# Performance work log

Measured on AMD Instinct MI355X. Metric: run time of the kernel, lower is better.

The kernel has to match this reference:

```python
import jax, jax.numpy as jnp
import numpy as np

N, E, C1, E2, C2, B = 30000, 400000, 15000, 100000, 7500, 16
FV, FE, NC = 6, 3, 10


def _lin(k, i, o):
    kw, kb = jax.random.split(k)
    s = 1.0 / np.sqrt(i)
    w = jax.random.uniform(kw, (i, o), jnp.float32, -s, s)
    b = jax.random.uniform(kb, (o,), jnp.float32, -s, s)
    return w, b


def setup_inputs() -> dict:
    key = jax.random.key(0)
    ks = jax.random.split(key, 20)
    inp = {}
    inp["x"] = jax.random.normal(ks[0], (N, FV), jnp.float32)
    inp["edge_attr"] = jax.random.uniform(ks[1], (E, FE), jnp.float32)
    inp["pos"] = jax.random.uniform(ks[2], (N, 3), jnp.float32)
    inp["edge_index"] = jax.random.randint(ks[3], (2, E), 0, N)
    inp["batch"] = jnp.sort(jax.random.randint(ks[4], (N,), 0, B))
    inp["cluster1"] = jax.random.randint(ks[5], (N,), 0, C1)
    inp["edge_index2"] = jax.random.randint(ks[6], (2, E2), 0, C1)
    inp["cluster2"] = jax.random.randint(ks[7], (C1,), 0, C2)
    inp["w1a"], inp["b1a"] = _lin(ks[8], FE, 25)
    inp["w1b"], inp["b1b"] = _lin(ks[9], 25, 32 * FV)
    inp["root1"] = jax.random.normal(ks[10], (FV, 32), jnp.float32) / np.sqrt(FV)
    inp["bias1"] = jnp.zeros((32,), jnp.float32)
    inp["w2a"], inp["b2a"] = _lin(ks[11], 3, 25)
    inp["w2b"], inp["b2b"] = _lin(ks[12], 25, 32 * 64)
    inp["root2"] = jax.random.normal(ks[13], (32, 64), jnp.float32) / np.sqrt(32)
    inp["bias2"] = jnp.zeros((64,), jnp.float32)
    inp["fc1_w"], inp["fc1_b"] = _lin(ks[14], 64, 128)
    inp["fc2_w"], inp["fc2_b"] = _lin(ks[15], 128, NC)
    return inp


def _seg_mean(v, idx, n):
    s = jax.ops.segment_sum(v, idx, num_segments=n)
    c = jax.ops.segment_sum(jnp.ones(idx.shape, v.dtype), idx, num_segments=n)
    return s / jnp.maximum(c, 1.0)[:, None]


def _seg_max(v, idx, n):
    m = jax.ops.segment_max(v, idx, num_segments=n)
    return jnp.where(jnp.isfinite(m), m, 0.0)  # empty clusters -> 0


def _nnconv(x, src, dst, ea, wa, ba, wb, bb, root, bias, n, ci, co):
    # per-edge weight matrix from edge MLP: [E, ci, co]
    W = (jax.nn.relu(ea @ wa + ba) @ wb + bb).reshape(-1, ci, co)
    msg = jnp.einsum('ei,eio->eo', x[src], W)  # gather + per-edge matmul
    return _seg_mean(msg, dst, n) + x @ root + bias  # scatter-mean + root


def _cartesian(pos, src, dst):
    cart = pos[src] - pos[dst]
    return cart / (2.0 * jnp.max(jnp.abs(cart))) + 0.5  # T.Cartesian(norm=True)


def reference(x, edge_attr, pos, w1a, b1a, w1b, b1b, root1, bias1,
              w2a, b2a, w2b, b2b, root2, bias2, fc1_w, fc1_b, fc2_w, fc2_b,
              edge_index, batch, cluster1, edge_index2, cluster2):
    src1, dst1 = edge_index[0], edge_index[1]
    x1 = jax.nn.elu(_nnconv(x, src1, dst1, edge_attr, w1a, b1a, w1b, b1b,
                            root1, bias1, N, FV, 32))
    # max_pool with precomputed graclus cluster assignment
    xp = _seg_max(x1, cluster1, C1)
    posp = _seg_mean(pos, cluster1, C1)
    batchp = jnp.maximum(jax.ops.segment_max(batch, cluster1, num_segments=C1), 0)
    src2, dst2 = edge_index2[0], edge_index2[1]
    ea2 = _cartesian(posp, src2, dst2)
    x2 = jax.nn.elu(_nnconv(xp, src2, dst2, ea2, w2a, b2a, w2b, b2b,
                            root2, bias2, C1, 32, 64))
    # max_pool_x with second cluster assignment
    x3 = _seg_max(x2, cluster2, C2)
    batch2 = jnp.maximum(jax.ops.segment_max(batchp, cluster2, num_segments=C2), 0)
    g = _seg_mean(x3, batch2, B)  # global mean pool -> [B, 64]
    h = jax.nn.elu(g @ fc1_w + fc1_b)
    # dropout is identity in eval mode
    return jax.nn.log_softmax(h @ fc2_w + fc2_b, axis=1)
```

## Files before the change

### kernel.cpp

```cpp
#include <hip/hip_runtime.h>
#include <hip/hip_bf16.h>

#define Nn 30000
#define Ee 400000
#define C1n 15000
#define E2n 100000
#define C2n 7500
#define Bb 16

#define OFF_SUM1   0
#define OFF_CNT1   960000
#define OFF_XPKEY  990000
#define OFF_POSSUM 1470000
#define OFF_CNTC1  1515000
#define OFF_BPMAX  1530000
#define OFF_SUM2   1545000
#define OFF_CNT2   2505000
#define OFF_X3KEY  2520000
#define OFF_B2MAX  3000000
#define OFF_GSUM   3007500
#define OFF_GCNT   3008524
#define OFF_MAXABS 3008540
#define ZERO_ELEMS 3008544
#define OFF_X1     3008544
#define OFF_XP     3968544
#define OFF_POSP   4448544
#define OFF_CART   4493544
#define OFF_H2     4793544
#define OFF_T2     7293544
#define OFF_X2     22653544

typedef __attribute__((ext_vector_type(8))) short short8;
typedef __attribute__((ext_vector_type(4))) float f32x4;

__device__ __forceinline__ unsigned fkey(float f) {
    unsigned u = __float_as_uint(f);
    return (u >> 31) ? ~u : (u | 0x80000000u);
}
__device__ __forceinline__ float funkey(unsigned k) {
    unsigned u = (k >> 31) ? (k ^ 0x80000000u) : ~k;
    return __uint_as_float(u);
}
__device__ __forceinline__ float elu(float a) { return a > 0.f ? a : expm1f(a); }

__device__ __forceinline__ unsigned short f2bf(float f) {
    unsigned u = __float_as_uint(f);
    unsigned lsb = (u >> 16) & 1u;
    u += 0x7fffu + lsb;
    return (unsigned short)(u >> 16);
}
__device__ __forceinline__ float bf2f(unsigned short s) {
    return __uint_as_float(((unsigned)s) << 16);
}

__global__ __launch_bounds__(256, 4) void conv1_mfma(
    const float* __restrict__ x, const float* __restrict__ ea,
    const int* __restrict__ ei,
    const float* __restrict__ w1a, const float* __restrict__ b1a,
    const float* __restrict__ w1b, const float* __restrict__ b1b,
    float* __restrict__ sum1, float* __restrict__ cnt1) {
    const int lane = threadIdx.x & 63;
    const int m = lane & 15;
    const int q = lane >> 4;

    short8 Bf[6][2];
#pragma unroll
    for (int s = 0; s < 6; ++s) {
#pragma unroll
        for (int h = 0; h < 2; ++h) {
            short8 pk;
#pragma unroll
            for (int j = 0; j < 8; ++j) {
                const int u = s * 8 + j;
                const int t = u / 6, i = u % 6;
                float w = 0.f;
                if (t < 7) {
                    int k = q + 4 * t;
                    int col = h * 16 + m;
                    if (k < 25)       w = w1b[k * 192 + i * 32 + col];
                    else if (k == 25) w = b1b[i * 32 + col];
                }
                pk[j] = (short)f2bf(w);
            }
            Bf[s][h] = pk;
        }
    }

    const int wid = (blockIdx.x * blockDim.x + threadIdx.x) >> 6;
    const int nw = (gridDim.x * blockDim.x) >> 6;
    for (int tile = wid; tile < Ee / 16; tile += nw) {
        const int e0 = tile * 16;
        const int e = e0 + m;
        const int src = ei[e];
        const float ea0 = ea[e * 3], ea1 = ea[e * 3 + 1], ea2 = ea[e * 3 + 2];
        float xs[6];
#pragma unroll
        for (int i = 0; i < 6; ++i) xs[i] = x[src * 6 + i];

        float hh[8];
#pragma unroll
        for (int t = 0; t < 6; ++t) {
            int k = q + 4 * t;
            float a = b1a[k] + ea0 * w1a[k] + ea1 * w1a[25 + k] + ea2 * w1a[50 + k];
            hh[t] = fmaxf(a, 0.f);
        }
        {
            if (q == 0) {
                float a = b1a[24] + ea0 * w1a[24] + ea1 * w1a[49] + ea2 * w1a[74];
                hh[6] = fmaxf(a, 0.f);
            } else hh[6] = (q == 1) ? 1.f : 0.f;
        }
        hh[7] = 0.f;

        f32x4 acc0 = {0.f, 0.f, 0.f, 0.f}, acc1 = {0.f, 0.f, 0.f, 0.f};
#pragma unroll
        for (int s = 0; s < 6; ++s) {
            short8 av;
#pragma unroll
            for (int j = 0; j < 8; ++j) {
                const int u = s * 8 + j;
                av[j] = (short)f2bf(hh[u / 6] * xs[u % 6]);
            }
            acc0 = __builtin_amdgcn_mfma_f32_16x16x32_bf16(av, Bf[s][0], acc0, 0, 0, 0);
            acc1 = __builtin_amdgcn_mfma_f32_16x16x32_bf16(av, Bf[s][1], acc1, 0, 0, 0);
        }

#pragma unroll
        for (int r = 0; r < 4; ++r) {
            const int row = q * 4 + r;
            const int dstr = ei[Ee + e0 + row];
            atomicAdd(&sum1[dstr * 32 + m], acc0[r]);
            atomicAdd(&sum1[dstr * 32 + 16 + m], acc1[r]);
        }
        if (q == 0) {
            const int dstm = ei[Ee + e0 + m];
            atomicAdd(&cnt1[dstm], 1.f);
        }
    }
}

__global__ void x1_kernel(const float* __restrict__ sum1, const float* __restrict__ cnt1,
                          const float* __restrict__ x, const float* __restrict__ root1,
                          const float* __restrict__ bias1, float* __restrict__ x1) {
    int t = blockIdx.x * 256 + threadIdx.x;
    if (t >= Nn * 32) return;
    int n = t >> 5, o = t & 31;
    float a = sum1[t] / fmaxf(cnt1[n], 1.f) + bias1[o];
#pragma unroll
    for (int i = 0; i < 6; ++i) a += x[n * 6 + i] * root1[i * 32 + o];
    x1[t] = elu(a);
}

__global__ void pool1_kernel(const float* __restrict__ x1, const float* __restrict__ pos,
                             const int* __restrict__ batch, const int* __restrict__ cluster1,
                             unsigned* __restrict__ xpkey, float* __restrict__ possum,
                             float* __restrict__ cntc1, int* __restrict__ bpmax) {
    int t = blockIdx.x * 256 + threadIdx.x;
    if (t >= Nn * 32) return;
    int n = t >> 5, o = t & 31;
    int c = cluster1[n];
    atomicMax(&xpkey[c * 32 + o], fkey(x1[t]));
    if (o == 0) {
#pragma unroll
        for (int j = 0; j < 3; ++j) atomicAdd(&possum[c * 3 + j], pos[n * 3 + j]);
        atomicAdd(&cntc1[c], 1.f);
        atomicMax(&bpmax[c], batch[n]);
    }
}

__global__ void pool1_final(const unsigned* __restrict__ xpkey, const float* __restrict__ possum,
                            const float* __restrict__ cntc1, float* __restrict__ xp,
                            float* __restrict__ posp) {
    int t = blockIdx.x * 256 + threadIdx.x;
    if (t >= C1n * 32) return;
    int c = t >> 5, o = t & 31;
    unsigned k = xpkey[t];
    xp[t] = k ? funkey(k) : 0.f;
    if (o < 3) posp[c * 3 + o] = possum[c * 3 + o] / fmaxf(cntc1[c], 1.f);
}

__global__ void cart_kernel(const float* __restrict__ posp, const int* __restrict__ ei2,
                            float* __restrict__ cart, unsigned* __restrict__ maxabs) {
    int e = blockIdx.x * 256 + threadIdx.x;
    float mx = 0.f;
    if (e < E2n) {
        int s = ei2[e], d = ei2[E2n + e];
#pragma unroll
        for (int j = 0; j < 3; ++j) {
            float cv = posp[s * 3 + j] - posp[d * 3 + j];
            cart[e * 3 + j] = cv;
            mx = fmaxf(mx, fabsf(cv));
        }
    }
#pragma unroll
    for (int off = 32; off > 0; off >>= 1) mx = fmaxf(mx, __shfl_xor(mx, off));
    if ((threadIdx.x & 63) == 0) atomicMax(maxabs, __float_as_uint(mx));
}

__global__ void h2_kernel(const float* __restrict__ cart, const unsigned* __restrict__ maxabs,
                          const float* __restrict__ w2a, const float* __restrict__ b2a,
                          float* __restrict__ h2) {
    int t = blockIdx.x * 256 + threadIdx.x;
    if (t >= E2n * 25) return;
    int e = t / 25, k = t % 25;
    float inv = 0.5f / __uint_as_float(maxabs[0]);
    float a = b2a[k];
#pragma unroll
    for (int j = 0; j < 3; ++j) a += (cart[e * 3 + j] * inv + 0.5f) * w2a[j * 25 + k];
    h2[t] = fmaxf(a, 0.f);
}

__global__ __launch_bounds__(256) void t2_gemm(const float* __restrict__ xp,
                                               const float* __restrict__ w2b,
                                               const float* __restrict__ b2b,
                                               unsigned short* __restrict__ T2) {
    __shared__ float As[256 * 36];
    __shared__ float Bs[32][68];
    const int bm = blockIdx.x * 256;
    const int bn = blockIdx.y * 64;
    const int t = threadIdx.x;
#pragma unroll
    for (int r = 0; r < 8; ++r) {
        int qd = t + r * 256;
        int row = qd >> 3, i4 = (qd & 7) * 4;
        int n = bm + row;
        float4 v = make_float4(0.f, 0.f, 0.f, 0.f);
        if (n < C1n) v = *reinterpret_cast<const float4*>(&xp[n * 32 + i4]);
        *reinterpret_cast<float4*>(&As[row * 36 + i4]) = v;
    }
#pragma unroll
    for (int r = 0; r < 8; ++r) {
        int idx = t + r * 256;
        int i = idx >> 6, nn = idx & 63;
        int col = bn + nn;
        int o = col >> 5, k = col & 31;
        float v = 0.f;
        if (k < 25)       v = w2b[k * 2048 + i * 64 + o];
        else if (k == 25) v = b2b[i * 64 + o];
        Bs[i][nn] = v;
    }
    __syncthreads();
    const int tn4 = (t & 15) * 4;
    const int tr = t >> 4;
    for (int it = 0; it < 8; ++it) {
        int r0 = it * 32 + tr, r1 = r0 + 16;
        float a0[32], a1[32];
#pragma unroll
        for (int qd = 0; qd < 8; ++qd) {
            *reinterpret_cast<float4*>(&a0[qd * 4]) = *reinterpret_cast<const float4*>(&As[r0 * 36 + qd * 4]);
            *reinterpret_cast<float4*>(&a1[qd * 4]) = *reinterpret_cast<const float4*>(&As[r1 * 36 + qd * 4]);
        }
        float acc0[4] = {0.f, 0.f, 0.f, 0.f}, acc1[4] = {0.f, 0.f, 0.f, 0.f};
#pragma unroll
        for (int k = 0; k < 32; ++k) {
            float4 bv = *reinterpret_cast<const float4*>(&Bs[k][tn4]);
            acc0[0] += a0[k] * bv.x; acc0[1] += a0[k] * bv.y;
            acc0[2] += a0[k] * bv.z; acc0[3] += a0[k] * bv.w;
            acc1[0] += a1[k] * bv.x; acc1[1] += a1[k] * bv.y;
            acc1[2] += a1[k] * bv.z; acc1[3] += a1[k] * bv.w;
        }
        int row0 = bm + r0, row1 = bm + r1;
        if (row0 < C1n) {
            union { unsigned short us[4]; uint2 v; } pk;
            pk.us[0] = f2bf(acc0[0]); pk.us[1] = f2bf(acc0[1]);
            pk.us[2] = f2bf(acc0[2]); pk.us[3] = f2bf(acc0[3]);
            *reinterpret_cast<uint2*>(&T2[(size_t)row0 * 2048 + bn + tn4]) = pk.v;
        }
        if (row1 < C1n) {
            union { unsigned short us[4]; uint2 v; } pk;
            pk.us[0] = f2bf(acc1[0]); pk.us[1] = f2bf(acc1[1]);
            pk.us[2] = f2bf(acc1[2]); pk.us[3] = f2bf(acc1[3]);
            *reinterpret_cast<uint2*>(&T2[(size_t)row1 * 2048 + bn + tn4]) = pk.v;
        }
    }
}

__global__ __launch_bounds__(256) void conv2_msg(
    const unsigned short* __restrict__ T2, const float* __restrict__ h2,
    const int* __restrict__ ei2, float* __restrict__ sum2, float* __restrict__ cnt2) {
    int t = blockIdx.x * 256 + threadIdx.x;
    if (t >= E2n * 64) return;
    int e = t >> 6, o = t & 63;
    int src = ei2[e], dst = ei2[E2n + e];
    const unsigned short* Tl = T2 + (size_t)src * 2048 + o * 32;
    uint4 a0 = *reinterpret_cast<const uint4*>(Tl);
    uint4 a1 = *reinterpret_cast<const uint4*>(Tl + 8);
    uint4 a2 = *reinterpret_cast<const uint4*>(Tl + 16);
    unsigned a3 = *reinterpret_cast<const unsigned*>(Tl + 24);
    float tv[26];
    unsigned w[13] = {a0.x, a0.y, a0.z, a0.w, a1.x, a1.y, a1.z, a1.w,
                      a2.x, a2.y, a2.z, a2.w, a3};
#pragma unroll
    for (int p = 0; p < 13; ++p) {
        tv[2 * p]     = __uint_as_float(w[p] << 16);
        tv[2 * p + 1] = __uint_as_float(w[p] & 0xffff0000u);
    }
    const float* he = h2 + e * 25;
    float acc = tv[25];
#pragma unroll
    for (int k = 0; k < 25; ++k) acc += he[k] * tv[k];
    atomicAdd(&sum2[dst * 64 + o], acc);
    if (o == 0) atomicAdd(&cnt2[dst], 1.f);
}

__global__ void x2_kernel(const float* __restrict__ sum2, const float* __restrict__ cnt2,
                          const float* __restrict__ xp, const float* __restrict__ root2,
                          const float* __restrict__ bias2, float* __restrict__ x2) {
    int t = blockIdx.x * 256 + threadIdx.x;
    if (t >= C1n * 64) return;
    int c = t >> 6, o = t & 63;
    float a = sum2[t] / fmaxf(cnt2[c], 1.f) + bias2[o];
#pragma unroll
    for (int i = 0; i < 32; ++i) a += xp[c * 32 + i] * root2[i * 64 + o];
    x2[t] = elu(a);
}

__global__ void pool2_kernel(const float* __restrict__ x2, const int* __restrict__ cluster2,
                             const int* __restrict__ bpmax, unsigned* __restrict__ x3key,
                             int* __restrict__ b2max) {
    int t = blockIdx.x * 256 + threadIdx.x;
    if (t >= C1n * 64) return;
    int c = t >> 6, o = t & 63;
    int c2 = cluster2[c];
    atomicMax(&x3key[c2 * 64 + o], fkey(x2[t]));
    if (o == 0) atomicMax(&b2max[c2], bpmax[c]);
}

__global__ __launch_bounds__(256) void gacc_kernel(
    const unsigned* __restrict__ x3key, const int* __restrict__ b2max,
    float* __restrict__ gsum, float* __restrict__ gcnt) {
    __shared__ float ls[Bb * 64];
    __shared__ float lc[Bb];
    const int t = threadIdx.x;
    for (int i = t; i < Bb * 64; i += 256) ls[i] = 0.f;
    if (t < Bb) lc[t] = 0.f;
    __syncthreads();
    const int o = t & 63;
    const int cs = t >> 6;
    for (int c = blockIdx.x * 4 + cs; c < C2n; c += gridDim.x * 4) {
        int b = b2max[c];
        unsigned k = x3key[c * 64 + o];
        float v = k ? funkey(k) : 0.f;
        atomicAdd(&ls[b * 64 + o], v);
        if (o == 0) atomicAdd(&lc[b], 1.f);
    }
    __syncthreads();
    for (int i = t; i < Bb * 64; i += 256) {
        float v = ls[i];
        if (v != 0.f) atomicAdd(&gsum[i], v);
    }
    if (t < Bb) {
        float v = lc[t];
        if (v != 0.f) atomicAdd(&gcnt[t], v);
    }
}

__global__ void head_kernel(const float* __restrict__ gsum, const float* __restrict__ gcnt,
                            const float* __restrict__ fc1w, const float* __restrict__ fc1b,
                            const float* __restrict__ fc2w, const float* __restrict__ fc2b,
                            float* __restrict__ out) {
    __shared__ float g[16 * 64];
    __shared__ float hb[16 * 128];
    __shared__ float lg[16 * 10];
    __shared__ float rowm[16];
    int t = threadIdx.x;
    for (int idx = t; idx < 16 * 64; idx += 256) {
        int b = idx >> 6;
        g[idx] = gsum[idx] / fmaxf(gcnt[b], 1.f);
    }
    __syncthreads();
    for (int idx = t; idx < 16 * 128; idx += 256) {
        int b = idx >> 7, j = idx & 127;
        float a = fc1b[j];
        for (int i = 0; i < 64; ++i) a += g[b * 64 + i] * fc1w[i * 128 + j];
        hb[idx] = elu(a);
    }
    __syncthreads();
    for (int idx = t; idx < 160; idx += 256) {
        int b = idx / 10, c = idx % 10;
        float a = fc2b[c];
        for (int i = 0; i < 128; ++i) a += hb[b * 128 + i] * fc2w[i * 10 + c];
        lg[idx] = a;
    }
    __syncthreads();
    if (t < 16) {
        float m = -1e30f;
        for (int c = 0; c < 10; ++c) m = fmaxf(m, lg[t * 10 + c]);
        float s = 0.f;
        for (int c = 0; c < 10; ++c) s += expf(lg[t * 10 + c] - m);
        rowm[t] = m + logf(s);
    }
    __syncthreads();
    for (int idx = t; idx < 160; idx += 256) out[idx] = lg[idx] - rowm[idx / 10];
}

extern "C" void kernel_launch(void* const* d_in, const int* in_sizes, int n_in,
                              void* d_out, int out_size, void* d_ws, size_t ws_size,
                              hipStream_t stream) {
    const float* x     = (const float*)d_in[0];
    const float* ea    = (const float*)d_in[1];
    const float* pos   = (const float*)d_in[2];
    const int*   ei    = (const int*)d_in[3];
    const int*   batch = (const int*)d_in[4];
    const int*   cl1   = (const int*)d_in[5];
    const int*   ei2   = (const int*)d_in[6];
    const int*   cl2   = (const int*)d_in[7];
    const float* w1a   = (const float*)d_in[8];
    const float* b1a   = (const float*)d_in[9];
    const float* w1b   = (const float*)d_in[10];
    const float* b1b   = (const float*)d_in[11];
    const float* root1 = (const float*)d_in[12];
    const float* bias1 = (const float*)d_in[13];
    const float* w2a   = (const float*)d_in[14];
    const float* b2a   = (const float*)d_in[15];
    const float* w2b   = (const float*)d_in[16];
    const float* b2b   = (const float*)d_in[17];
    const float* root2 = (const float*)d_in[18];
    const float* bias2 = (const float*)d_in[19];
    const float* fc1w  = (const float*)d_in[20];
    const float* fc1b  = (const float*)d_in[21];
    const float* fc2w  = (const float*)d_in[22];
    const float* fc2b  = (const float*)d_in[23];
    float* out = (float*)d_out;

    float* ws = (float*)d_ws;
    float*    sum1   = ws + OFF_SUM1;
    float*    cnt1   = ws + OFF_CNT1;
    unsigned* xpkey  = (unsigned*)(ws + OFF_XPKEY);
    float*    possum = ws + OFF_POSSUM;
    float*    cntc1  = ws + OFF_CNTC1;
    int*      bpmax  = (int*)(ws + OFF_BPMAX);
    float*    sum2   = ws + OFF_SUM2;
    float*    cnt2   = ws + OFF_CNT2;
    unsigned* x3key  = (unsigned*)(ws + OFF_X3KEY);
    int*      b2max  = (int*)(ws + OFF_B2MAX);
    float*    gsum   = ws + OFF_GSUM;
    float*    gcnt   = ws + OFF_GCNT;
    unsigned* maxabs = (unsigned*)(ws + OFF_MAXABS);
    float*    x1     = ws + OFF_X1;
    float*    xp     = ws + OFF_XP;
    float*    posp   = ws + OFF_POSP;
    float*    cart   = ws + OFF_CART;
    float*    h2     = ws + OFF_H2;
    unsigned short* T2 = (unsigned short*)(ws + OFF_T2);
    float*    x2     = ws + OFF_X2;

    hipMemsetAsync(ws, 0, (size_t)ZERO_ELEMS * 4, stream);

    conv1_mfma<<<2048, 256, 0, stream>>>(x, ea, ei, w1a, b1a, w1b, b1b, sum1, cnt1);
    x1_kernel<<<(Nn * 32 + 255) / 256, 256, 0, stream>>>(sum1, cnt1, x, root1, bias1, x1);
    pool1_kernel<<<(Nn * 32 + 255) / 256, 256, 0, stream>>>(x1, pos, batch, cl1, xpkey, possum, cntc1, bpmax);
    pool1_final<<<(C1n * 32 + 255) / 256, 256, 0, stream>>>(xpkey, possum, cntc1, xp, posp);
    cart_kernel<<<(E2n + 255) / 256, 256, 0, stream>>>(posp, ei2, cart, maxabs);
    h2_kernel<<<(E2n * 25 + 255) / 256, 256, 0, stream>>>(cart, maxabs, w2a, b2a, h2);
    dim3 tgrid((C1n + 255) / 256, 2048 / 64);
    t2_gemm<<<tgrid, 256, 0, stream>>>(xp, w2b, b2b, T2);
    conv2_msg<<<(E2n * 64 + 255) / 256, 256, 0, stream>>>(T2, h2, ei2, sum2, cnt2);
    x2_kernel<<<(C1n * 64 + 255) / 256, 256, 0, stream>>>(sum2, cnt2, xp, root2, bias2, x2);
    pool2_kernel<<<(C1n * 64 + 255) / 256, 256, 0, stream>>>(x2, cl2, bpmax, x3key, b2max);
    gacc_kernel<<<32, 256, 0, stream>>>(x3key, b2max, gsum, gcnt);
    head_kernel<<<1, 256, 0, stream>>>(gsum, gcnt, fc1w, fc1b, fc2w, fc2b, out);
}
```

Measured before the change: 373.6 us.

## Sort conv1 edges by destination and merge runs before atomic scatter

Adds a counting sort of the 400k conv1 edges by destination: a histogram, a single-block scan and an atomic-cursor scatter build a permutation and a sorted destination array. conv1 then processes edges in sorted order and merges consecutive rows with the same destination before issuing atomics. This removes the per-edge count atomics, because the count now comes from the CSR offsets. The aim is fewer contended atomics in the scatter-mean. In exchange it adds three kernels, including a serial single-block scan over 30k entries, and gathers of source nodes and edge attributes become indirect through the permutation. With an average of about 13 edges per node, merging runs of 4 rows only modestly reduces the number of atomics.

```diff
diff --git a/kernel.cpp b/kernel.cpp
--- a/kernel.cpp
+++ b/kernel.cpp
@@ -9,7 +9,7 @@
 #define Bb 16
 
 #define OFF_SUM1   0
-#define OFF_CNT1   960000
+#define OFF_HIST   960000
 #define OFF_XPKEY  990000
 #define OFF_POSSUM 1470000
 #define OFF_CNTC1  1515000
@@ -29,6 +29,10 @@
 #define OFF_H2     4793544
 #define OFF_T2     7293544
 #define OFF_X2     22653544
+#define OFF_OFFS   23613544
+#define OFF_CURSOR 23643545
+#define OFF_PERM   23673545
+#define OFF_DSTS   24073545
 
 typedef __attribute__((ext_vector_type(8))) short short8;
 typedef __attribute__((ext_vector_type(4))) float f32x4;
@@ -53,12 +57,55 @@
     return __uint_as_float(((unsigned)s) << 16);
 }
 
+__global__ void hist_kernel(const int* __restrict__ ei, unsigned* __restrict__ hist) {
+    int e = blockIdx.x * 256 + threadIdx.x;
+    if (e < Ee) atomicAdd(&hist[ei[Ee + e]], 1u);
+}
+
+__global__ __launch_bounds__(1024) void scan_kernel(const unsigned* __restrict__ hist,
+                                                    unsigned* __restrict__ offs,
+                                                    unsigned* __restrict__ cursor) {
+    __shared__ unsigned tmp[1024];
+    __shared__ unsigned carry;
+    if (threadIdx.x == 0) carry = 0u;
+    __syncthreads();
+    for (int base = 0; base < Nn; base += 1024) {
+        int i = base + threadIdx.x;
+        unsigned v = (i < Nn) ? hist[i] : 0u;
+        tmp[threadIdx.x] = v;
+        __syncthreads();
+        for (int d = 1; d < 1024; d <<= 1) {
+            unsigned t = (threadIdx.x >= (unsigned)d) ? tmp[threadIdx.x - d] : 0u;
+            __syncthreads();
+            tmp[threadIdx.x] += t;
+            __syncthreads();
+        }
+        unsigned excl = tmp[threadIdx.x] - v + carry;
+        if (i < Nn) { offs[i] = excl; cursor[i] = excl; }
+        __syncthreads();
+        if (threadIdx.x == 0) carry += tmp[1023];
+        __syncthreads();
+    }
+    if (threadIdx.x == 0) offs[Nn] = Ee;
+}
+
+__global__ void scatter_kernel(const int* __restrict__ ei, unsigned* __restrict__ cursor,
+                               unsigned* __restrict__ perm, int* __restrict__ dsts) {
+    int e = blockIdx.x * 256 + threadIdx.x;
+    if (e >= Ee) return;
+    int d = ei[Ee + e];
+    unsigned p = atomicAdd(&cursor[d], 1u);
+    perm[p] = (unsigned)e;
+    dsts[p] = d;
+}
+
 __global__ __launch_bounds__(256, 4) void conv1_mfma(
     const float* __restrict__ x, const float* __restrict__ ea,
-    const int* __restrict__ ei,
+    const int* __restrict__ ei, const unsigned* __restrict__ perm,
+    const int* __restrict__ dsts,
     const float* __restrict__ w1a, const float* __restrict__ b1a,
     const float* __restrict__ w1b, const float* __restrict__ b1b,
-    float* __restrict__ sum1, float* __restrict__ cnt1) {
+    float* __restrict__ sum1) {
     const int lane = threadIdx.x & 63;
     const int m = lane & 15;
     const int q = lane >> 4;
@@ -90,7 +137,7 @@
     const int nw = (gridDim.x * blockDim.x) >> 6;
     for (int tile = wid; tile < Ee / 16; tile += nw) {
         const int e0 = tile * 16;
-        const int e = e0 + m;
+        const int e = (int)perm[e0 + m];
         const int src = ei[e];
         const float ea0 = ea[e * 3], ea1 = ea[e * 3 + 1], ea2 = ea[e * 3 + 2];
         float xs[6];
@@ -125,27 +172,41 @@
             acc1 = __builtin_amdgcn_mfma_f32_16x16x32_bf16(av, Bf[s][1], acc1, 0, 0, 0);
         }
 
-#pragma unroll
-        for (int r = 0; r < 4; ++r) {
-            const int row = q * 4 + r;
-            const int dstr = ei[Ee + e0 + row];
-            atomicAdd(&sum1[dstr * 32 + m], acc0[r]);
-            atomicAdd(&sum1[dstr * 32 + 16 + m], acc1[r]);
-        }
-        if (q == 0) {
-            const int dstm = ei[Ee + e0 + m];
-            atomicAdd(&cnt1[dstm], 1.f);
-        }
-    }
-}
-
-__global__ void x1_kernel(const float* __restrict__ sum1, const float* __restrict__ cnt1,
+        const int rb = e0 + q * 4;
+        const int d0 = dsts[rb], d1 = dsts[rb + 1], d2 = dsts[rb + 2], d3 = dsts[rb + 3];
+        float s0 = acc0[0], s1 = acc1[0];
+        int dp = d0;
+        if (d1 == dp) { s0 += acc0[1]; s1 += acc1[1]; }
+        else {
+            atomicAdd(&sum1[dp * 32 + m], s0);
+            atomicAdd(&sum1[dp * 32 + 16 + m], s1);
+            s0 = acc0[1]; s1 = acc1[1]; dp = d1;
+        }
+        if (d2 == dp) { s0 += acc0[2]; s1 += acc1[2]; }
+        else {
+            atomicAdd(&sum1[dp * 32 + m], s0);
+            atomicAdd(&sum1[dp * 32 + 16 + m], s1);
+            s0 = acc0[2]; s1 = acc1[2]; dp = d2;
+        }
+        if (d3 == dp) { s0 += acc0[3]; s1 += acc1[3]; }
+        else {
+            atomicAdd(&sum1[dp * 32 + m], s0);
+            atomicAdd(&sum1[dp * 32 + 16 + m], s1);
+            s0 = acc0[3]; s1 = acc1[3]; dp = d3;
+        }
+        atomicAdd(&sum1[dp * 32 + m], s0);
+        atomicAdd(&sum1[dp * 32 + 16 + m], s1);
+    }
+}
+
+__global__ void x1_kernel(const float* __restrict__ sum1, const unsigned* __restrict__ offs,
                           const float* __restrict__ x, const float* __restrict__ root1,
                           const float* __restrict__ bias1, float* __restrict__ x1) {
     int t = blockIdx.x * 256 + threadIdx.x;
     if (t >= Nn * 32) return;
     int n = t >> 5, o = t & 31;
-    float a = sum1[t] / fmaxf(cnt1[n], 1.f) + bias1[o];
+    float c = (float)(offs[n + 1] - offs[n]);
+    float a = sum1[t] / fmaxf(c, 1.f) + bias1[o];
 #pragma unroll
     for (int i = 0; i < 6; ++i) a += x[n * 6 + i] * root1[i * 32 + o];
     x1[t] = elu(a);
@@ -425,7 +486,7 @@
 
     float* ws = (float*)d_ws;
     float*    sum1   = ws + OFF_SUM1;
-    float*    cnt1   = ws + OFF_CNT1;
+    unsigned* hist   = (unsigned*)(ws + OFF_HIST);
     unsigned* xpkey  = (unsigned*)(ws + OFF_XPKEY);
     float*    possum = ws + OFF_POSSUM;
     float*    cntc1  = ws + OFF_CNTC1;
@@ -444,11 +505,18 @@
     float*    h2     = ws + OFF_H2;
     unsigned short* T2 = (unsigned short*)(ws + OFF_T2);
     float*    x2     = ws + OFF_X2;
+    unsigned* offs   = (unsigned*)(ws + OFF_OFFS);
+    unsigned* cursor = (unsigned*)(ws + OFF_CURSOR);
+    unsigned* perm   = (unsigned*)(ws + OFF_PERM);
+    int*      dsts   = (int*)(ws + OFF_DSTS);
 
     hipMemsetAsync(ws, 0, (size_t)ZERO_ELEMS * 4, stream);
 
-    conv1_mfma<<<2048, 256, 0, stream>>>(x, ea, ei, w1a, b1a, w1b, b1b, sum1, cnt1);
-    x1_kernel<<<(Nn * 32 + 255) / 256, 256, 0, stream>>>(sum1, cnt1, x, root1, bias1, x1);
+    hist_kernel<<<(Ee + 255) / 256, 256, 0, stream>>>(ei, hist);
+    scan_kernel<<<1, 1024, 0, stream>>>(hist, offs, cursor);
+    scatter_kernel<<<(Ee + 255) / 256, 256, 0, stream>>>(ei, cursor, perm, dsts);
+    conv1_mfma<<<2048, 256, 0, stream>>>(x, ea, ei, perm, dsts, w1a, b1a, w1b, b1b, sum1);
+    x1_kernel<<<(Nn * 32 + 255) / 256, 256, 0, stream>>>(sum1, offs, x, root1, bias1, x1);
     pool1_kernel<<<(Nn * 32 + 255) / 256, 256, 0, stream>>>(x1, pos, batch, cl1, xpkey, possum, cntc1, bpmax);
     pool1_final<<<(C1n * 32 + 255) / 256, 256, 0, stream>>>(xpkey, possum, cntc1, xp, posp);
     cart_kernel<<<(E2n + 255) / 256, 256, 0, stream>>>(posp, ei2, cart, maxabs);
```

Result: slower. 446.7 us (+19.6%).
